# Kernel tuning notes

Hardware: AMD Instinct MI355X
Metric: run time of the kernel (lower is better)

The kernel has to match this reference:

```python
import jax, jax.numpy as jnp
import numpy as np

B = 128
J = 22
Q = J * 4          # 88
R = 3
C = 4
H = 512            # LSTM hidden
ENC = 256 * 3      # 768 concatenated encoder outputs
STATE_IN = Q + R + C   # 95
OFF_IN = Q + R         # 91
OUT = Q + R + C        # 95


def _linear_params(key, fan_in, fan_out):
    kw, kb = jax.random.split(key)
    s = 1.0 / np.sqrt(fan_in)
    w = jax.random.uniform(kw, (fan_in, fan_out), jnp.float32, -s, s)
    b = jax.random.uniform(kb, (fan_out,), jnp.float32, -s, s)
    return w, b


def setup_inputs() -> dict:
    key = jax.random.key(0)
    ks = jax.random.split(key, 24)
    inp = {
        "past_root_vel": jax.random.normal(ks[0], (B, 10, R)) * 0.1,
        "past_quats": jax.random.normal(ks[1], (B, 10, Q)),
        "past_root_offset": jax.random.normal(ks[2], (B, 10, R)),
        "past_quat_offset": jax.random.normal(ks[3], (B, 10, Q)),
        "past_contacts": jax.random.uniform(ks[4], (B, 10, C)),
        "target_root_pos": jax.random.normal(ks[5], (B, R)),
        "target_quats": jax.random.normal(ks[6], (B, Q)),
        "init_root_pos": jax.random.normal(ks[7], (B, R)),
        "pred_weights": jax.random.normal(ks[8], (B, 4 * H, ENC + H)) * 0.03,
        "pred_bias": jax.random.normal(ks[9], (B, 4 * H)) * 0.01,
    }
    inp["se_w1"], inp["se_b1"] = _linear_params(ks[10], STATE_IN, 512)
    inp["se_w2"], inp["se_b2"] = _linear_params(ks[11], 512, 256)
    inp["oe_w1"], inp["oe_b1"] = _linear_params(ks[12], OFF_IN, 512)
    inp["oe_w2"], inp["oe_b2"] = _linear_params(ks[13], 512, 256)
    inp["te_w1"], inp["te_b1"] = _linear_params(ks[14], Q, 512)
    inp["te_w2"], inp["te_b2"] = _linear_params(ks[15], 512, 256)
    inp["de_w1"], inp["de_b1"] = _linear_params(ks[16], H, 512)
    inp["de_w2"], inp["de_b2"] = _linear_params(ks[17], 512, 256)
    inp["de_w3"], inp["de_b3"] = _linear_params(ks[18], 256, OUT)
    return inp


def reference(past_root_vel, past_quats, past_root_offset, past_quat_offset,
              past_contacts, target_root_pos, target_quats, init_root_pos,
              pred_weights, pred_bias,
              se_w1, se_b1, se_w2, se_b2,
              oe_w1, oe_b1, oe_w2, oe_b2,
              te_w1, te_b1, te_w2, te_b2,
              de_w1, de_b1, de_w2, de_b2, de_w3, de_b3):
    b = past_quats.shape[0]

    def enc(x, w1, b1, w2, b2):
        return jax.nn.relu(jax.nn.relu(x @ w1 + b1) @ w2 + b2)

    # target encoding is identical every step; hoist it
    h_target = enc(target_quats, te_w1, te_b1, te_w2, te_b2)

    def step(root_vel, quats, root_offset, quat_offset, contacts, h, c):
        state_vec = jnp.concatenate([contacts, quats, root_vel], axis=1)
        offset_vec = jnp.concatenate([root_offset, quat_offset], axis=1)
        h_state = enc(state_vec, se_w1, se_b1, se_w2, se_b2)
        h_offset = enc(offset_vec, oe_w1, oe_b1, oe_w2, oe_b2)
        pred_in = jnp.concatenate([h_state, h_offset, h_target], axis=1)  # [B,768]
        # per-sample hypernetwork LSTM cell (torch gate order i,f,g,o)
        z = jnp.concatenate([pred_in, h], axis=1)  # [B, 1280]
        gates = jnp.einsum('boi,bi->bo', pred_weights, z) + pred_bias
        i_g, f_g, g_g, o_g = jnp.split(gates, 4, axis=1)
        c2 = jax.nn.sigmoid(f_g) * c + jax.nn.sigmoid(i_g) * jnp.tanh(g_g)
        h2 = jax.nn.sigmoid(o_g) * jnp.tanh(c2)
        # decoder (512,512,256,out), no activation on last layer
        d = jax.nn.relu(h2 @ de_w1 + de_b1)
        d = jax.nn.relu(d @ de_w2 + de_b2)
        out = d @ de_w3 + de_b3
        next_quats = out[:, :Q] + quats
        next_rvel = out[:, Q:Q + R] + root_vel
        next_contacts = jax.nn.sigmoid(out[:, Q + R:])
        nq = next_quats.reshape(b, Q // 4, 4)
        nq = nq / jnp.maximum(jnp.linalg.norm(nq, axis=2, keepdims=True), 1e-12)
        return next_rvel, nq.reshape(b, Q), next_contacts, h2, c2

    h0 = jnp.zeros((b, H), past_quats.dtype)
    c0 = jnp.zeros((b, H), past_quats.dtype)

    def past_body(carry, x):
        glob, h, c, _, _, _, _, _ = carry
        rvel, quats, roff, qoff, cont = x
        nrv, nq, nc, h2, c2 = step(rvel, quats, roff, qoff, cont, h, c)
        glob2 = glob + rvel
        nroff = glob2 - target_root_pos
        nqoff = nq - target_quats
        return (glob2, h2, c2, nrv, nq, nc, nroff, nqoff), None

    z3 = jnp.zeros((b, R), past_quats.dtype)
    init = (init_root_pos, h0, c0, z3,
            jnp.zeros((b, Q), past_quats.dtype),
            jnp.zeros((b, C), past_quats.dtype),
            z3, jnp.zeros((b, Q), past_quats.dtype))
    xs = (jnp.swapaxes(past_root_vel, 0, 1), jnp.swapaxes(past_quats, 0, 1),
          jnp.swapaxes(past_root_offset, 0, 1), jnp.swapaxes(past_quat_offset, 0, 1),
          jnp.swapaxes(past_contacts, 0, 1))
    carry, _ = jax.lax.scan(past_body, init, xs)
    glob, h, c, nrv, nq, nc, roff, qoff = carry

    first_frame = jnp.concatenate([nrv, nq], axis=1)  # NOTE: rvel not glob, as in source

    def trans_body(carry, _):
        glob, h, c, rvel, quats, cont, roff, qoff = carry
        nrv, nq, nc, h2, c2 = step(rvel, quats, roff, qoff, cont, h, c)
        glob2 = glob + nrv
        nroff = glob2 - target_root_pos
        nqoff = nq - target_quats
        pose = jnp.concatenate([glob2, nq], axis=1)
        return (glob2, h2, c2, nrv, nq, nc, nroff, nqoff), (pose, nc)

    carry2 = (glob, h, c, nrv, nq, nc, roff, qoff)
    _, (poses, conts) = jax.lax.scan(trans_body, carry2, None, length=29)

    pred_poses = jnp.concatenate([first_frame[:, None], jnp.swapaxes(poses, 0, 1)], axis=1)
    pred_contacts = jnp.concatenate([nc[:, None], jnp.swapaxes(conts, 0, 1)], axis=1)
    return pred_poses, pred_contacts
```

## Files before the change

kernel.cpp:

```cpp
#include <hip/hip_runtime.h>
#include <hip/hip_bf16.h>
#include <math.h>

#define BATCH 128
#define QD 88
#define HDIM 512
#define ZDIM 1280
#define GDIM 2048
#define PROW 1024
#define QSTRIDE 4096
#define NPAST 10
#define NTRANS 29
#define NSTEPS (NPAST + NTRANS)
#define OUTD 95
#define POSE_ELEMS (BATCH * 30 * 91)

typedef float f32x4 __attribute__((ext_vector_type(4)));
typedef unsigned int u32x4 __attribute__((ext_vector_type(4)));

__device__ __forceinline__ float sig_(float x) { return 1.0f / (1.0f + expf(-x)); }
__device__ __forceinline__ void dot4_(const u32x4 wv, const float4 zv, float& d) {
    const float4 f = *(const float4*)&wv;
    d = fmaf(f.x, zv.x, d); d = fmaf(f.y, zv.y, d);
    d = fmaf(f.z, zv.z, d); d = fmaf(f.w, zv.w, d);
}
__device__ __forceinline__ void dot4u_(const uint4 wv, const float4 zv, float& d) {
    const float4 f = *(const float4*)&wv;
    d = fmaf(f.x, zv.x, d); d = fmaf(f.y, zv.y, d);
    d = fmaf(f.z, zv.z, d); d = fmaf(f.w, zv.w, d);
}
__device__ __forceinline__ void fma4_(float4& acc, float x, const float4 w) {
    acc.x = fmaf(x, w.x, acc.x); acc.y = fmaf(x, w.y, acc.y);
    acc.z = fmaf(x, w.z, acc.z); acc.w = fmaf(x, w.w, acc.w);
}
__device__ __forceinline__ unsigned q8_(float w, float inv) {
    const unsigned u = __float2uint_rn(fmaf(w, inv, 128.0f));
    return (u > 255u) ? 255u : u;
}
__device__ __forceinline__ unsigned pack8_(const u32x4 a, float inv) {
    return q8_(__uint_as_float(a.x), inv) | (q8_(__uint_as_float(a.y), inv) << 8)
         | (q8_(__uint_as_float(a.z), inv) << 16) | (q8_(__uint_as_float(a.w), inv) << 24);
}
__device__ __forceinline__ float d8_(unsigned d, const float4 z) {
    float acc = 0.f;
    acc = fmaf((float)((int)(d & 0xFFu) - 128), z.x, acc);
    acc = fmaf((float)((int)((d >> 8) & 0xFFu) - 128), z.y, acc);
    acc = fmaf((float)((int)((d >> 16) & 0xFFu) - 128), z.z, acc);
    acc = fmaf((float)((int)(d >> 24) - 128), z.w, acc);
    return acc;
}
__device__ __forceinline__ float wredmax_(float m) {
    #pragma unroll
    for (int s = 32; s >= 1; s >>= 1) m = fmaxf(m, __shfl_xor(m, s, 64));
    return m;
}
__device__ __forceinline__ float amax4_(const u32x4 a, float m) {
    m = fmaxf(m, fabsf(__uint_as_float(a.x))); m = fmaxf(m, fabsf(__uint_as_float(a.y)));
    m = fmaxf(m, fabsf(__uint_as_float(a.z))); m = fmaxf(m, fabsf(__uint_as_float(a.w)));
    return m;
}

__global__ void __launch_bounds__(256)
matvec0_conv(const float* __restrict__ W, const float* __restrict__ z_ws,
             const float* __restrict__ pred_bias, unsigned char* __restrict__ Wp,
             float* __restrict__ scale_ws, float* __restrict__ g_ws, float* __restrict__ g0_ws)
{
    const int b = blockIdx.x >> 5, chunk = blockIdx.x & 31;
    const int wave = threadIdx.x >> 6, lane = threadIdx.x & 63;
    const int row0 = chunk * 64 + wave * 16;
    const float* zb = z_ws + b * ZDIM;
    const float biasv = (lane < 16) ? pred_bias[b * GDIM + row0 + lane] : 0.f;
    const int l4 = lane * 4;
    const float4 z0 = *(const float4*)(zb + l4);
    const float4 z1 = *(const float4*)(zb + 256 + l4);
    const float4 zh = *(const float4*)(zb + 512 + l4);
    const float4 z3 = *(const float4*)(zb + 768 + l4);
    const float4 z4 = *(const float4*)(zb + 1024 + l4);
    const char* wb = (const char*)W + (size_t)b * GDIM * ZDIM * 4;
    char* dstB = (char*)Wp + (size_t)b * GDIM * PROW;

    #define ISSUE(p, B) { const char* a_ = wb + (size_t)(row0 + 2 * (p)) * (ZDIM * 4) + lane * 16; \
        _Pragma("unroll") for (int i = 0; i < 10; ++i) \
            B[i] = __builtin_nontemporal_load((const u32x4*)(a_ + i * 1024)); }

    u32x4 bufa[10], bufb[10];
    ISSUE(0, bufa);
    #pragma unroll
    for (int p = 0; p < 8; ++p) {
        u32x4* cur = (p & 1) ? bufb : bufa;
        u32x4* nxt = (p & 1) ? bufa : bufb;
        if (p < 7) ISSUE(p + 1, nxt);
        float dynA = 0.f, dynB = 0.f, statA = 0.f, statB = 0.f;
        dot4_(cur[0], z0, dynA); dot4_(cur[1], z1, dynA);
        dot4_(cur[2], zh, statA);
        dot4_(cur[3], z3, dynA); dot4_(cur[4], z4, dynA);
        dot4_(cur[5], z0, dynB); dot4_(cur[6], z1, dynB);
        dot4_(cur[7], zh, statB);
        dot4_(cur[8], z3, dynB); dot4_(cur[9], z4, dynB);
        float m0 = 0.f, m1 = 0.f;
        m0 = amax4_(cur[0], m0); m0 = amax4_(cur[1], m0);
        m0 = amax4_(cur[3], m0); m0 = amax4_(cur[4], m0);
        m1 = amax4_(cur[5], m1); m1 = amax4_(cur[6], m1);
        m1 = amax4_(cur[8], m1); m1 = amax4_(cur[9], m1);
        m0 = wredmax_(m0); m1 = wredmax_(m1);
        const float s0 = m0 * (1.f / 127.f), s1 = m1 * (1.f / 127.f);
        const float inv0 = (m0 > 0.f) ? 127.f / m0 : 0.f;
        const float inv1 = (m1 > 0.f) ? 127.f / m1 : 0.f;
        {
            const int rp = row0 + 2 * p;
            char* base = dstB + (size_t)(rp >> 2) * QSTRIDE + (size_t)((rp >> 1) & 1) * 1024
                       + lane * 16;
            u32x4 v;
            v.x = pack8_(cur[0], inv0); v.y = pack8_(cur[1], inv0);
            v.z = pack8_(cur[5], inv1); v.w = pack8_(cur[6], inv1);
            __builtin_nontemporal_store(v, (u32x4*)(base));
            v.x = pack8_(cur[3], inv0); v.y = pack8_(cur[4], inv0);
            v.z = pack8_(cur[8], inv1); v.w = pack8_(cur[9], inv1);
            __builtin_nontemporal_store(v, (u32x4*)(base + 2048));
        }
        if (lane == 0) { scale_ws[b * GDIM + row0 + 2 * p] = s0;
                         scale_ws[b * GDIM + row0 + 2 * p + 1] = s1; }
        float sd0 = dynA + __shfl_xor(dynA, 32);
        float sd1 = dynB + __shfl_xor(dynB, 32);
        float ud = (lane < 32) ? sd0 : sd1;
        float ss0 = statA + __shfl_xor(statA, 32);
        float ss1 = statB + __shfl_xor(statB, 32);
        float us = (lane < 32) ? ss0 : ss1;
        #pragma unroll
        for (int m = 16; m >= 1; m >>= 1) { ud += __shfl_xor(ud, m); us += __shfl_xor(us, m); }
        const float badd = __shfl(biasv, 2 * p + ((lane >= 32) ? 1 : 0), 64);
        if (lane == 0 || lane == 32) {
            const int r = row0 + 2 * p + ((lane >= 32) ? 1 : 0);
            g0_ws[b * GDIM + r] = us + badd;
            g_ws[b * GDIM + r]  = ud + us + badd;
        }
    }
    #undef ISSUE
}

__device__ __forceinline__ void redwrite_(float rA, float rB, int lane,
                                          float g0v, float scv, int idx0,
                                          float* __restrict__ dst, int drow0) {
    const float sA = rA + __shfl_xor(rA, 32);
    const float sB = rB + __shfl_xor(rB, 32);
    float u = (lane < 32) ? sA : sB;
    #pragma unroll
    for (int m = 16; m >= 1; m >>= 1) u += __shfl_xor(u, m);
    const int hilo = (lane >= 32) ? 1 : 0;
    const float badd = __shfl(g0v, idx0 + hilo, 64);
    const float srow = __shfl(scv, idx0 + hilo, 64);
    const float val = badd + srow * u;
    if (lane == 0)       dst[drow0] = val;
    else if (lane == 32) dst[drow0 + 1] = val;
}

__global__ void __launch_bounds__(256)
epass(const unsigned char* __restrict__ Wp, const float* __restrict__ enc9,
      const float* __restrict__ scale_ws, const float* __restrict__ g0_ws,
      float* __restrict__ E_ws)
{
    const int b = blockIdx.x >> 5, chunk = blockIdx.x & 31;
    const int wave = threadIdx.x >> 6, lane = threadIdx.x & 63;
    const int row0 = chunk * 64 + wave * 16;
    const int q0 = row0 >> 2;
    const int l4 = lane * 4;
    float4 eA[9], eB[9];
    #pragma unroll
    for (int s = 0; s < 9; ++s) {
        const float* eb = enc9 + ((size_t)s * BATCH + b) * 512;
        eA[s] = *(const float4*)(eb + l4);
        eB[s] = *(const float4*)(eb + 256 + l4);
    }
    const float g0v = (lane < 16) ? g0_ws[b * GDIM + row0 + lane] : 0.f;
    const float scv = (lane < 16) ? scale_ws[b * GDIM + row0 + lane] : 0.f;
    const char* wb = (const char*)Wp + (size_t)b * GDIM * PROW;

    #define ISSUE(qq, B) { const char* a_ = wb + (size_t)(q0 + (qq)) * QSTRIDE + lane * 16; \
        B[0] = __builtin_nontemporal_load((const u32x4*)(a_)); \
        B[1] = __builtin_nontemporal_load((const u32x4*)(a_ + 1024)); }

    u32x4 bufa[2], bufb[2];
    ISSUE(0, bufa);
    #pragma unroll
    for (int qq = 0; qq < 4; ++qq) {
        u32x4* cur = (qq & 1) ? bufb : bufa;
        u32x4* nxt = (qq & 1) ? bufa : bufb;
        if (qq < 3) ISSUE(qq + 1, nxt);
        #pragma unroll
        for (int s = 0; s < 9; ++s) {
            const float r0 = d8_(cur[0].x, eA[s]) + d8_(cur[0].y, eB[s]);
            const float r1 = d8_(cur[0].z, eA[s]) + d8_(cur[0].w, eB[s]);
            const float r2 = d8_(cur[1].x, eA[s]) + d8_(cur[1].y, eB[s]);
            const float r3 = d8_(cur[1].z, eA[s]) + d8_(cur[1].w, eB[s]);
            float* dst = E_ws + ((size_t)s * BATCH + b) * GDIM;
            redwrite_(r0, r1, lane, g0v, scv, 4 * qq,     dst, row0 + 4 * qq);
            redwrite_(r2, r3, lane, g0v, scv, 4 * qq + 2, dst, row0 + 4 * qq + 2);
        }
    }
    #undef ISSUE
}

__global__ void __launch_bounds__(256)
matvecH(const unsigned char* __restrict__ Wp, const float* __restrict__ z_ws,
        const float* __restrict__ scale_ws, const float* __restrict__ Es,
        float* __restrict__ g_ws)
{
    const int b = blockIdx.x >> 5, chunk = blockIdx.x & 31;
    const int wave = threadIdx.x >> 6, lane = threadIdx.x & 63;
    const int row0 = chunk * 64 + wave * 16;
    const int q0 = row0 >> 2;
    const float* zb = z_ws + b * ZDIM;
    const int l4 = lane * 4;
    const float4 z3 = *(const float4*)(zb + 768 + l4);
    const float4 z4 = *(const float4*)(zb + 1024 + l4);
    const float Ev  = (lane < 16) ? Es[b * GDIM + row0 + lane] : 0.f;
    const float scv = (lane < 16) ? scale_ws[b * GDIM + row0 + lane] : 0.f;
    const char* wb = (const char*)Wp + (size_t)b * GDIM * PROW;

    #define ISSUE(qq, B) { const char* a_ = wb + (size_t)(q0 + (qq)) * QSTRIDE + 2048 + lane * 16; \
        B[0] = *(const u32x4*)(a_); \
        B[1] = *(const u32x4*)(a_ + 1024); }

    u32x4 buf0[2], buf1[2], buf2[2];
    ISSUE(0, buf0);
    ISSUE(1, buf1);
    #pragma unroll
    for (int qq = 0; qq < 4; ++qq) {
        u32x4* cur = (qq % 3 == 0) ? buf0 : (qq % 3 == 1) ? buf1 : buf2;
        u32x4* nxt = ((qq + 2) % 3 == 0) ? buf0 : ((qq + 2) % 3 == 1) ? buf1 : buf2;
        if (qq < 2) ISSUE(qq + 2, nxt);
        const float r0 = d8_(cur[0].x, z3) + d8_(cur[0].y, z4);
        const float r1 = d8_(cur[0].z, z3) + d8_(cur[0].w, z4);
        const float r2 = d8_(cur[1].x, z3) + d8_(cur[1].y, z4);
        const float r3 = d8_(cur[1].z, z3) + d8_(cur[1].w, z4);
        float* dst = g_ws + b * GDIM;
        redwrite_(r0, r1, lane, Ev, scv, 4 * qq,     dst, row0 + 4 * qq);
        redwrite_(r2, r3, lane, Ev, scv, 4 * qq + 2, dst, row0 + 4 * qq + 2);
    }
    #undef ISSUE
}

__global__ void __launch_bounds__(256)
matvec8(const unsigned char* __restrict__ Wp, const float* __restrict__ z_ws,
        const float* __restrict__ scale_ws, const float* __restrict__ g0_ws,
        float* __restrict__ g_ws)
{
    const int b = blockIdx.x >> 5, chunk = blockIdx.x & 31;
    const int wave = threadIdx.x >> 6, lane = threadIdx.x & 63;
    const int row0 = chunk * 64 + wave * 16;
    const int q0 = row0 >> 2;
    const float* zb = z_ws + b * ZDIM;
    const int l4 = lane * 4;
    const float4 z0 = *(const float4*)(zb + l4);
    const float4 z1 = *(const float4*)(zb + 256 + l4);
    const float4 z3 = *(const float4*)(zb + 768 + l4);
    const float4 z4 = *(const float4*)(zb + 1024 + l4);
    const float g0v = (lane < 16) ? g0_ws[b * GDIM + row0 + lane] : 0.f;
    const float scv = (lane < 16) ? scale_ws[b * GDIM + row0 + lane] : 0.f;
    const char* wb = (const char*)Wp + (size_t)b * GDIM * PROW;

    #define ISSUE(qq, B) { const char* a_ = wb + (size_t)(q0 + (qq)) * QSTRIDE + lane * 16; \
        B[0] = __builtin_nontemporal_load((const u32x4*)(a_)); \
        B[1] = __builtin_nontemporal_load((const u32x4*)(a_ + 1024)); \
        B[2] = __builtin_nontemporal_load((const u32x4*)(a_ + 2048)); \
        B[3] = __builtin_nontemporal_load((const u32x4*)(a_ + 3072)); }

    u32x4 buf0[4], buf1[4], buf2[4];
    ISSUE(0, buf0);
    ISSUE(1, buf1);
    #pragma unroll
    for (int qq = 0; qq < 4; ++qq) {
        u32x4* cur = (qq % 3 == 0) ? buf0 : (qq % 3 == 1) ? buf1 : buf2;
        u32x4* nxt = ((qq + 2) % 3 == 0) ? buf0 : ((qq + 2) % 3 == 1) ? buf1 : buf2;
        if (qq < 2) ISSUE(qq + 2, nxt);
        const float r0 = d8_(cur[0].x, z0) + d8_(cur[0].y, z1)
                       + d8_(cur[2].x, z3) + d8_(cur[2].y, z4);
        const float r1 = d8_(cur[0].z, z0) + d8_(cur[0].w, z1)
                       + d8_(cur[2].z, z3) + d8_(cur[2].w, z4);
        const float r2 = d8_(cur[1].x, z0) + d8_(cur[1].y, z1)
                       + d8_(cur[3].x, z3) + d8_(cur[3].y, z4);
        const float r3 = d8_(cur[1].z, z0) + d8_(cur[1].w, z1)
                       + d8_(cur[3].z, z3) + d8_(cur[3].w, z4);
        float* dst = g_ws + b * GDIM;
        redwrite_(r0, r1, lane, g0v, scv, 4 * qq,     dst, row0 + 4 * qq);
        redwrite_(r2, r3, lane, g0v, scv, 4 * qq + 2, dst, row0 + 4 * qq + 2);
    }
    #undef ISSUE
}

__global__ void __launch_bounds__(512)
lstmk(const float* __restrict__ g_ws, float* __restrict__ z_ws, float* __restrict__ c_ws)
{
    const int b = blockIdx.x, t = threadIdx.x;
    const float* g = g_ws + b * GDIM;
    const float ig = g[t], fg = g[512 + t], gg = g[1024 + t], og = g[1536 + t];
    const float c2 = sig_(fg) * c_ws[b * HDIM + t] + sig_(ig) * tanhf(gg);
    c_ws[b * HDIM + t] = c2;
    z_ws[b * ZDIM + 768 + t] = sig_(og) * tanhf(c2);
}

__global__ void __launch_bounds__(512)
initk(const float* __restrict__ past_root_vel, const float* __restrict__ past_quats,
      const float* __restrict__ past_root_offset, const float* __restrict__ past_quat_offset,
      const float* __restrict__ past_contacts, const float* __restrict__ target_quats,
      const float* __restrict__ init_root_pos,
      const float* __restrict__ se_w1, const float* __restrict__ se_b1,
      const float* __restrict__ se_w2, const float* __restrict__ se_b2,
      const float* __restrict__ oe_w1, const float* __restrict__ oe_b1,
      const float* __restrict__ oe_w2, const float* __restrict__ oe_b2,
      const float* __restrict__ te_w1, const float* __restrict__ te_b1,
      const float* __restrict__ te_w2, const float* __restrict__ te_b2,
      float* __restrict__ z_ws, float* __restrict__ c_ws, float* __restrict__ car_ws)
{
    const int b = blockIdx.x, t = threadIdx.x;
    __shared__ float tq[QD], bufA[512], bufB[512], sv[95], ov[91];

    if (t < 192) {
        float v = 0.f;
        if (t < 3) {
            v = init_root_pos[b * 3 + t];
            for (int s = 0; s < NPAST - 1; ++s) v += past_root_vel[(b * NPAST + s) * 3 + t];
        }
        car_ws[b * 192 + t] = v;
    }
    c_ws[b * HDIM + t] = 0.f;
    z_ws[b * ZDIM + 768 + t] = 0.f;
    if (t < QD) tq[t] = target_quats[b * QD + t];
    if (t < 4)  sv[t] = past_contacts[b * NPAST * 4 + t];
    if (t < QD) { sv[4 + t] = past_quats[b * NPAST * QD + t];
                  ov[3 + t] = past_quat_offset[b * NPAST * QD + t]; }
    if (t < 3)  { sv[92 + t] = past_root_vel[b * NPAST * 3 + t];
                  ov[t]      = past_root_offset[b * NPAST * 3 + t]; }
    __syncthreads();
    {
        float a = te_b1[t];
        #pragma unroll 8
        for (int i = 0; i < QD; ++i) a = fmaf(tq[i], te_w1[i * 512 + t], a);
        bufA[t] = fmaxf(a, 0.f);
    }
    __syncthreads();
    if (t < 256) {
        float a = te_b2[t];
        #pragma unroll 8
        for (int i = 0; i < 512; ++i) a = fmaf(bufA[i], te_w2[i * 256 + t], a);
        z_ws[b * ZDIM + 512 + t] = fmaxf(a, 0.f);
    }
    __syncthreads();
    {
        float aS = se_b1[t], aO = oe_b1[t];
        #pragma unroll 8
        for (int i = 0; i < 91; ++i) { aS = fmaf(sv[i], se_w1[i * 512 + t], aS);
                                       aO = fmaf(ov[i], oe_w1[i * 512 + t], aO); }
        #pragma unroll
        for (int i = 91; i < 95; ++i) aS = fmaf(sv[i], se_w1[i * 512 + t], aS);
        bufA[t] = fmaxf(aS, 0.f);
        bufB[t] = fmaxf(aO, 0.f);
    }
    __syncthreads();
    if (t < 256) {
        float a = se_b2[t];
        #pragma unroll 8
        for (int i = 0; i < 512; ++i) a = fmaf(bufA[i], se_w2[i * 256 + t], a);
        z_ws[b * ZDIM + t] = fmaxf(a, 0.f);
    } else {
        const int j = t - 256;
        float a = oe_b2[j];
        #pragma unroll 8
        for (int i = 0; i < 512; ++i) a = fmaf(bufB[i], oe_w2[i * 256 + j], a);
        z_ws[b * ZDIM + 256 + j] = fmaxf(a, 0.f);
    }
}

__global__ void __launch_bounds__(512)
enc_past(const float* __restrict__ past_root_vel, const float* __restrict__ past_quats,
         const float* __restrict__ past_root_offset, const float* __restrict__ past_quat_offset,
         const float* __restrict__ past_contacts,
         const float* __restrict__ se_w1, const float* __restrict__ se_b1,
         const float* __restrict__ se_w2, const float* __restrict__ se_b2,
         const float* __restrict__ oe_w1, const float* __restrict__ oe_b1,
         const float* __restrict__ oe_w2, const float* __restrict__ oe_b2,
         float* __restrict__ enc9)
{
    const int b = blockIdx.x, t = threadIdx.x;
    const int s = blockIdx.y + 1;
    __shared__ float bufA[512], bufB[512], sv[95], ov[91];

    if (t < 4)  sv[t] = past_contacts[(b * NPAST + s) * 4 + t];
    if (t < QD) { sv[4 + t] = past_quats[(b * NPAST + s) * QD + t];
                  ov[3 + t] = past_quat_offset[(b * NPAST + s) * QD + t]; }
    if (t < 3)  { sv[92 + t] = past_root_vel[(b * NPAST + s) * 3 + t];
                  ov[t]      = past_root_offset[(b * NPAST + s) * 3 + t]; }
    __syncthreads();
    {
        float aS = se_b1[t], aO = oe_b1[t];
        #pragma unroll 8
        for (int i = 0; i < 91; ++i) { aS = fmaf(sv[i], se_w1[i * 512 + t], aS);
                                       aO = fmaf(ov[i], oe_w1[i * 512 + t], aO); }
        #pragma unroll
        for (int i = 91; i < 95; ++i) aS = fmaf(sv[i], se_w1[i * 512 + t], aS);
        bufA[t] = fmaxf(aS, 0.f);
        bufB[t] = fmaxf(aO, 0.f);
    }
    __syncthreads();
    float* dst = enc9 + ((size_t)(s - 1) * BATCH + b) * 512;
    if (t < 256) {
        float a = se_b2[t];
        #pragma unroll 8
        for (int i = 0; i < 512; ++i) a = fmaf(bufA[i], se_w2[i * 256 + t], a);
        dst[t] = fmaxf(a, 0.f);
    } else {
        const int j = t - 256;
        float a = oe_b2[j];
        #pragma unroll 8
        for (int i = 0; i < 512; ++i) a = fmaf(bufB[i], oe_w2[i * 256 + j], a);
        dst[256 + j] = fmaxf(a, 0.f);
    }
}

__global__ void __launch_bounds__(512)
stepk(const float* __restrict__ past_root_vel, const float* __restrict__ past_quats,
      const float* __restrict__ past_root_offset, const float* __restrict__ past_quat_offset,
      const float* __restrict__ past_contacts, const float* __restrict__ target_root_pos,
      const float* __restrict__ target_quats,
      const float* __restrict__ se_w1, const float* __restrict__ se_b1,
      const float* __restrict__ se_w2, const float* __restrict__ se_b2,
      const float* __restrict__ oe_w1, const float* __restrict__ oe_b1,
      const float* __restrict__ oe_w2, const float* __restrict__ oe_b2,
      const float* __restrict__ de_w1, const float* __restrict__ de_b1,
      const float* __restrict__ de_w2, const float* __restrict__ de_b2,
      const float* __restrict__ de_w3, const float* __restrict__ de_b3,
      float* __restrict__ out, float* __restrict__ z_ws, const float* __restrict__ g_ws,
      float* __restrict__ c_ws, float* __restrict__ car_ws, int s, int skip_enc)
{
    const int b = blockIdx.x, t = threadIdx.x;
    __shared__ float4 part4[512];
    __shared__ __align__(16) float h2s[HDIM], bufA[512], bufB[512], d2[256];
    __shared__ float outv[OUTD], nq[QD], sv[95], ov[91], carryL[192], tq[QD], trp[3];
    __shared__ float rvn[3], globn[3], contn[4];

    if (t < 192) carryL[t] = car_ws[b * 192 + t];
    if (t < QD) tq[t] = target_quats[b * QD + t];
    if (t < 3)  trp[t] = target_root_pos[b * 3 + t];

    {
        const float* g = g_ws + b * GDIM;
        const float ig = g[t], fg = g[512 + t], gg = g[1024 + t], og = g[1536 + t];
        const float c2 = sig_(fg) * c_ws[b * HDIM + t] + sig_(ig) * tanhf(gg);
        c_ws[b * HDIM + t] = c2;
        const float h2 = sig_(og) * tanhf(c2);
        h2s[t] = h2;
        z_ws[b * ZDIM + 768 + t] = h2;
    }
    __syncthreads();
    {
        const int c = t & 127, s4 = t >> 7;
        float4 acc = {0.f, 0.f, 0.f, 0.f};
        const float* w = de_w1 + (size_t)(s4 * 128) * 512 + 4 * c;
        #pragma unroll 8
        for (int k = 0; k < 128; ++k)
            fma4_(acc, h2s[s4 * 128 + k], *(const float4*)(w + (size_t)k * 512));
        part4[t] = acc;
    }
    __syncthreads();
    if (t < 128) {
        float4 v = part4[t];
        #pragma unroll
        for (int s4 = 1; s4 < 4; ++s4) { const float4 p = part4[s4 * 128 + t];
            v.x += p.x; v.y += p.y; v.z += p.z; v.w += p.w; }
        const float4 bb = *(const float4*)(de_b1 + 4 * t);
        float4 r; r.x = fmaxf(v.x + bb.x, 0.f); r.y = fmaxf(v.y + bb.y, 0.f);
        r.z = fmaxf(v.z + bb.z, 0.f); r.w = fmaxf(v.w + bb.w, 0.f);
        *(float4*)&bufA[4 * t] = r;
    }
    __syncthreads();
    {
        const int c = t & 63, s8 = t >> 6;
        float4 acc = {0.f, 0.f, 0.f, 0.f};
        const float* w = de_w2 + (size_t)(s8 * 64) * 256 + 4 * c;
        #pragma unroll 8
        for (int k = 0; k < 64; ++k)
            fma4_(acc, bufA[s8 * 64 + k], *(const float4*)(w + (size_t)k * 256));
        part4[t] = acc;
    }
    __syncthreads();
    if (t < 64) {
        float4 v = part4[t];
        #pragma unroll
        for (int s8 = 1; s8 < 8; ++s8) { const float4 p = part4[s8 * 64 + t];
            v.x += p.x; v.y += p.y; v.z += p.z; v.w += p.w; }
        const float4 bb = *(const float4*)(de_b2 + 4 * t);
        float4 r; r.x = fmaxf(v.x + bb.x, 0.f); r.y = fmaxf(v.y + bb.y, 0.f);
        r.z = fmaxf(v.z + bb.z, 0.f); r.w = fmaxf(v.w + bb.w, 0.f);
        *(float4*)&d2[4 * t] = r;
    }
    __syncthreads();
    if (t < OUTD) {
        float acc = de_b3[t];
        #pragma unroll 16
        for (int i = 0; i < 256; ++i) acc = fmaf(d2[i], de_w3[i * OUTD + t], acc);
        outv[t] = acc;
    }
    __syncthreads();

    const bool pastS = (s < NPAST);
    if (t < QD) {
        const float qin = pastS ? past_quats[(b * NPAST + s) * QD + t] : carryL[10 + t];
        nq[t] = outv[t] + qin;
    }
    __syncthreads();
    if (t < 22) {
        const float a = nq[4 * t], b2 = nq[4 * t + 1], c3 = nq[4 * t + 2], d4 = nq[4 * t + 3];
        const float inv = 1.f / fmaxf(sqrtf(a * a + b2 * b2 + c3 * c3 + d4 * d4), 1e-12f);
        nq[4 * t] = a * inv; nq[4 * t + 1] = b2 * inv; nq[4 * t + 2] = c3 * inv; nq[4 * t + 3] = d4 * inv;
    }
    if (t < 3) {
        const float rin = pastS ? past_root_vel[(b * NPAST + s) * 3 + t] : carryL[3 + t];
        const float nrv = outv[88 + t] + rin;
        const float g = carryL[t] + (pastS ? rin : nrv);
        rvn[t] = nrv; globn[t] = g;
    }
    if (t < 4) contn[t] = sig_(outv[91 + t]);
    __syncthreads();

    if (t < 3) { car_ws[b * 192 + t] = globn[t]; car_ws[b * 192 + 3 + t] = rvn[t];
                 car_ws[b * 192 + 186 + t] = globn[t] - trp[t]; }
    if (t < 4) car_ws[b * 192 + 6 + t] = contn[t];
    if (t < QD) { car_ws[b * 192 + 10 + t] = nq[t]; car_ws[b * 192 + 98 + t] = nq[t] - tq[t]; }
    if (s == NPAST - 1) {
        const size_t pb = (size_t)b * 30 * 91;
        if (t < 3)  out[pb + t] = rvn[t];
        if (t < QD) out[pb + 3 + t] = nq[t];
        if (t < 4)  out[POSE_ELEMS + (size_t)b * 30 * 4 + t] = contn[t];
    } else if (!pastS) {
        const int k = s - NPAST + 1;
        const size_t pb = ((size_t)b * 30 + k) * 91;
        if (t < 3)  out[pb + t] = globn[t];
        if (t < QD) out[pb + 3 + t] = nq[t];
        if (t < 4)  out[POSE_ELEMS + ((size_t)b * 30 + k) * 4 + t] = contn[t];
    }
    if (s == NSTEPS - 1) return;
    if (skip_enc) return;

    const int nx = s + 1;
    if (nx < NPAST) {
        if (t < 4)  sv[t] = past_contacts[(b * NPAST + nx) * 4 + t];
        if (t < QD) { sv[4 + t] = past_quats[(b * NPAST + nx) * QD + t];
                      ov[3 + t] = past_quat_offset[(b * NPAST + nx) * QD + t]; }
        if (t < 3)  { sv[92 + t] = past_root_vel[(b * NPAST + nx) * 3 + t];
                      ov[t]      = past_root_offset[(b * NPAST + nx) * 3 + t]; }
    } else {
        if (t < 4)  sv[t] = contn[t];
        if (t < QD) { sv[4 + t] = nq[t]; ov[3 + t] = nq[t] - tq[t]; }
        if (t < 3)  { sv[92 + t] = rvn[t]; ov[t] = globn[t] - trp[t]; }
    }
    __syncthreads();
    {
        const int tt = t & 255, enc = t >> 8;
        const int c = tt & 127, sl = tt >> 7;
        const float* inp = enc ? ov : sv;
        const float* w1  = enc ? oe_w1 : se_w1;
        const int nin  = enc ? 91 : 95;
        const int half = enc ? 46 : 48;
        const int i0 = sl * half;
        const int iend = (i0 + half < nin) ? (i0 + half) : nin;
        float4 acc = {0.f, 0.f, 0.f, 0.f};
        #pragma unroll 8
        for (int k = 0; k < 48; ++k) {
            const int i = i0 + k;
            if (i < iend) fma4_(acc, inp[i], *(const float4*)(w1 + (size_t)i * 512 + 4 * c));
        }
        part4[enc * 256 + tt] = acc;
    }
    __syncthreads();
    if (t < 128) {
        const float4 a = part4[t], b2 = part4[128 + t];
        const float4 bb = *(const float4*)(se_b1 + 4 * t);
        float4 r; r.x = fmaxf(a.x + b2.x + bb.x, 0.f); r.y = fmaxf(a.y + b2.y + bb.y, 0.f);
        r.z = fmaxf(a.z + b2.z + bb.z, 0.f); r.w = fmaxf(a.w + b2.w + bb.w, 0.f);
        *(float4*)&bufA[4 * t] = r;
    } else if (t < 256) {
        const int c = t - 128;
        const float4 a = part4[256 + c], b2 = part4[384 + c];
        const float4 bb = *(const float4*)(oe_b1 + 4 * c);
        float4 r; r.x = fmaxf(a.x + b2.x + bb.x, 0.f); r.y = fmaxf(a.y + b2.y + bb.y, 0.f);
        r.z = fmaxf(a.z + b2.z + bb.z, 0.f); r.w = fmaxf(a.w + b2.w + bb.w, 0.f);
        *(float4*)&bufB[4 * c] = r;
    }
    __syncthreads();
    {
        const int tt = t & 255, enc = t >> 8;
        const int c = tt & 63, sl = tt >> 6;
        const float* inp = enc ? bufB : bufA;
        const float* w2  = enc ? oe_w2 : se_w2;
        float4 acc = {0.f, 0.f, 0.f, 0.f};
        const float* w = w2 + (size_t)(sl * 128) * 256 + 4 * c;
        #pragma unroll 8
        for (int k = 0; k < 128; ++k)
            fma4_(acc, inp[sl * 128 + k], *(const float4*)(w + (size_t)k * 256));
        part4[enc * 256 + tt] = acc;
    }
    __syncthreads();
    if (t < 64) {
        float4 v = part4[t];
        #pragma unroll
        for (int sl = 1; sl < 4; ++sl) { const float4 p = part4[sl * 64 + t];
            v.x += p.x; v.y += p.y; v.z += p.z; v.w += p.w; }
        const float4 bb = *(const float4*)(se_b2 + 4 * t);
        float4 r; r.x = fmaxf(v.x + bb.x, 0.f); r.y = fmaxf(v.y + bb.y, 0.f);
        r.z = fmaxf(v.z + bb.z, 0.f); r.w = fmaxf(v.w + bb.w, 0.f);
        *(float4*)(z_ws + b * ZDIM + 4 * t) = r;
    } else if (t < 128) {
        const int c = t - 64;
        float4 v = part4[256 + c];
        #pragma unroll
        for (int sl = 1; sl < 4; ++sl) { const float4 p = part4[256 + sl * 64 + c];
            v.x += p.x; v.y += p.y; v.z += p.z; v.w += p.w; }
        const float4 bb = *(const float4*)(oe_b2 + 4 * c);
        float4 r; r.x = fmaxf(v.x + bb.x, 0.f); r.y = fmaxf(v.y + bb.y, 0.f);
        r.z = fmaxf(v.z + bb.z, 0.f); r.w = fmaxf(v.w + bb.w, 0.f);
        *(float4*)(z_ws + b * ZDIM + 256 + 4 * c) = r;
    }
}

__global__ void __launch_bounds__(256)
matvec_f32(const float* __restrict__ W, const float* __restrict__ z_ws,
           const float* __restrict__ pred_bias, float* __restrict__ g_ws)
{
    const int b = blockIdx.x >> 5, chunk = blockIdx.x & 31;
    const int wave = threadIdx.x >> 6, lane = threadIdx.x & 63;
    const int row0 = chunk * 64 + wave * 16;
    const float* zb = z_ws + b * ZDIM;
    const float biasv = (lane < 16) ? pred_bias[b * GDIM + row0 + lane] : 0.f;
    const int l4 = lane * 4;
    const float4 z0 = *(const float4*)(zb + l4);
    const float4 z1 = *(const float4*)(zb + 256 + l4);
    const float4 z2 = *(const float4*)(zb + 512 + l4);
    const float4 z3 = *(const float4*)(zb + 768 + l4);
    const float4 z4 = *(const float4*)(zb + 1024 + l4);
    const char* wb = (const char*)W + (size_t)b * GDIM * ZDIM * 4;

    #define ISSUE(p, B) { const char* a_ = wb + (size_t)(row0 + 2 * (p)) * (ZDIM * 4) + lane * 16; \
        _Pragma("unroll") for (int i = 0; i < 10; ++i) B[i] = *(const uint4*)(a_ + i * 1024); }

    uint4 bufa[10], bufb[10];
    ISSUE(0, bufa);
    #pragma unroll
    for (int p = 0; p < 8; ++p) {
        uint4* cur = (p & 1) ? bufb : bufa;
        uint4* nxt = (p & 1) ? bufa : bufb;
        if (p < 7) ISSUE(p + 1, nxt);
        float accA = 0.f, accB = 0.f;
        dot4u_(cur[0], z0, accA); dot4u_(cur[1], z1, accA); dot4u_(cur[2], z2, accA);
        dot4u_(cur[3], z3, accA); dot4u_(cur[4], z4, accA);
        dot4u_(cur[5], z0, accB); dot4u_(cur[6], z1, accB); dot4u_(cur[7], z2, accB);
        dot4u_(cur[8], z3, accB); dot4u_(cur[9], z4, accB);
        float s0 = accA + __shfl_xor(accA, 32);
        float s1 = accB + __shfl_xor(accB, 32);
        float u = (lane < 32) ? s0 : s1;
        #pragma unroll
        for (int m = 16; m >= 1; m >>= 1) u += __shfl_xor(u, m);
        const float badd = __shfl(biasv, 2 * p + ((lane >= 32) ? 1 : 0), 64);
        if (lane == 0)       g_ws[b * GDIM + row0 + 2 * p]     = u + badd;
        else if (lane == 32) g_ws[b * GDIM + row0 + 2 * p + 1] = u + badd;
    }
    #undef ISSUE
}

extern "C" void kernel_launch(void* const* d_in, const int* in_sizes, int n_in,
                              void* d_out, int out_size, void* d_ws, size_t ws_size,
                              hipStream_t stream) {
    const float* prv = (const float*)d_in[0];
    const float* pq  = (const float*)d_in[1];
    const float* pro = (const float*)d_in[2];
    const float* pqo = (const float*)d_in[3];
    const float* pc  = (const float*)d_in[4];
    const float* trp = (const float*)d_in[5];
    const float* tq  = (const float*)d_in[6];
    const float* irp = (const float*)d_in[7];
    const float* pw  = (const float*)d_in[8];
    const float* pb  = (const float*)d_in[9];
    const float* se_w1 = (const float*)d_in[10]; const float* se_b1 = (const float*)d_in[11];
    const float* se_w2 = (const float*)d_in[12]; const float* se_b2 = (const float*)d_in[13];
    const float* oe_w1 = (const float*)d_in[14]; const float* oe_b1 = (const float*)d_in[15];
    const float* oe_w2 = (const float*)d_in[16]; const float* oe_b2 = (const float*)d_in[17];
    const float* te_w1 = (const float*)d_in[18]; const float* te_b1 = (const float*)d_in[19];
    const float* te_w2 = (const float*)d_in[20]; const float* te_b2 = (const float*)d_in[21];
    const float* de_w1 = (const float*)d_in[22]; const float* de_b1 = (const float*)d_in[23];
    const float* de_w2 = (const float*)d_in[24]; const float* de_b2 = (const float*)d_in[25];
    const float* de_w3 = (const float*)d_in[26]; const float* de_b3 = (const float*)d_in[27];
    float* outp = (float*)d_out;

    const size_t WPACKB = (size_t)BATCH * GDIM * PROW;
    const size_t AUXB = (size_t)BATCH * (GDIM * 3 + ZDIM + HDIM + 192) * 4
                      + (size_t)9 * BATCH * 512 * 4
                      + (size_t)9 * BATCH * GDIM * 4;
    const bool bf = ws_size >= WPACKB + AUXB;

    char* base = (char*)d_ws;
    float* scale_ws; float* g0_ws; float* z_ws;
    if (bf) {
        scale_ws = (float*)(base + WPACKB);
        g0_ws    = scale_ws + (size_t)BATCH * GDIM;
        z_ws     = g0_ws + (size_t)BATCH * GDIM;
    } else {
        scale_ws = nullptr;
        g0_ws    = nullptr;
        z_ws     = (float*)base;
    }
    float* g_ws    = z_ws + (size_t)BATCH * ZDIM;
    float* c_ws    = g_ws + (size_t)BATCH * GDIM;
    float* car_ws  = c_ws + (size_t)BATCH * HDIM;
    float* enc9_ws = car_ws + (size_t)BATCH * 192;
    float* E_ws    = enc9_ws + (size_t)9 * BATCH * 512;

    initk<<<dim3(BATCH), dim3(512), 0, stream>>>(prv, pq, pro, pqo, pc, tq, irp,
        se_w1, se_b1, se_w2, se_b2, oe_w1, oe_b1, oe_w2, oe_b2,
        te_w1, te_b1, te_w2, te_b2, z_ws, c_ws, car_ws);

    if (bf) {
        enc_past<<<dim3(BATCH, 9), dim3(512), 0, stream>>>(prv, pq, pro, pqo, pc,
            se_w1, se_b1, se_w2, se_b2, oe_w1, oe_b1, oe_w2, oe_b2, enc9_ws);
        matvec0_conv<<<dim3(BATCH * 32), dim3(256), 0, stream>>>(
            pw, z_ws, pb, (unsigned char*)d_ws, scale_ws, g_ws, g0_ws);
        epass<<<dim3(BATCH * 32), dim3(256), 0, stream>>>(
            (const unsigned char*)d_ws, enc9_ws, scale_ws, g0_ws, E_ws);
        for (int s = 0; s < NSTEPS; ++s) {
            if (s >= 1 && s < NPAST) {
                matvecH<<<dim3(BATCH * 32), dim3(256), 0, stream>>>(
                    (const unsigned char*)d_ws, z_ws, scale_ws,
                    E_ws + (size_t)(s - 1) * BATCH * GDIM, g_ws);
            } else if (s >= NPAST) {
                matvec8<<<dim3(BATCH * 32), dim3(256), 0, stream>>>(
                    (const unsigned char*)d_ws, z_ws, scale_ws, g0_ws, g_ws);
            }
            if (s < NPAST - 1) {
                lstmk<<<dim3(BATCH), dim3(512), 0, stream>>>(g_ws, z_ws, c_ws);
            } else {
                stepk<<<dim3(BATCH), dim3(512), 0, stream>>>(prv, pq, pro, pqo, pc, trp, tq,
                    se_w1, se_b1, se_w2, se_b2, oe_w1, oe_b1, oe_w2, oe_b2,
                    de_w1, de_b1, de_w2, de_b2, de_w3, de_b3,
                    outp, z_ws, g_ws, c_ws, car_ws, s, 0);
            }
        }
    } else {
        for (int s = 0; s < NSTEPS; ++s) {
            matvec_f32<<<dim3(BATCH * 32), dim3(256), 0, stream>>>(pw, z_ws, pb, g_ws);
            stepk<<<dim3(BATCH), dim3(512), 0, stream>>>(prv, pq, pro, pqo, pc, trp, tq,
                se_w1, se_b1, se_w2, se_b2, oe_w1, oe_b1, oe_w2, oe_b2,
                de_w1, de_b1, de_w2, de_b2, de_w3, de_b3,
                outp, z_ws, g_ws, c_ws, car_ws, s, 0);
        }
    }
}
```

Before: 3.418 ms.

## Split transition matvec into hidden and state parts, overlap decoder tail with hidden matvec

In the transition phase, the single fused matvec over the state, offset and hidden parts is split in two. The hidden-state part (matvecH, writing partial gates to a scratch buffer) runs in the same launch as the per-batch decoder/encoder tail (bck). A smaller matvecS then adds the state-encoder contribution once the tail has produced the new encodings. The intent is to take the decoder MLP and state-encoder work off the serial critical path by running it concurrently with the large weight stream, at the cost of an extra launch per step and a read/write of the partial gate buffer. matvecH loads also switch to nontemporal.

```diff
diff --git a/kernel.cpp b/kernel.cpp
--- a/kernel.cpp
+++ b/kernel.cpp
@@ -200,13 +200,14 @@
     #undef ISSUE
 }
 
-__global__ void __launch_bounds__(256)
-matvecH(const unsigned char* __restrict__ Wp, const float* __restrict__ z_ws,
-        const float* __restrict__ scale_ws, const float* __restrict__ Es,
-        float* __restrict__ g_ws)
-{
-    const int b = blockIdx.x >> 5, chunk = blockIdx.x & 31;
-    const int wave = threadIdx.x >> 6, lane = threadIdx.x & 63;
+__device__ __forceinline__ void mvH_body_(int blk, const unsigned char* __restrict__ Wp,
+                                          const float* __restrict__ z_ws,
+                                          const float* __restrict__ scale_ws,
+                                          const float* __restrict__ Es,
+                                          float* __restrict__ dstg, int tid)
+{
+    const int b = blk >> 5, chunk = blk & 31;
+    const int wave = tid >> 6, lane = tid & 63;
     const int row0 = chunk * 64 + wave * 16;
     const int q0 = row0 >> 2;
     const float* zb = z_ws + b * ZDIM;
@@ -218,8 +219,8 @@
     const char* wb = (const char*)Wp + (size_t)b * GDIM * PROW;
 
     #define ISSUE(qq, B) { const char* a_ = wb + (size_t)(q0 + (qq)) * QSTRIDE + 2048 + lane * 16; \
-        B[0] = *(const u32x4*)(a_); \
-        B[1] = *(const u32x4*)(a_ + 1024); }
+        B[0] = __builtin_nontemporal_load((const u32x4*)(a_)); \
+        B[1] = __builtin_nontemporal_load((const u32x4*)(a_ + 1024)); }
 
     u32x4 buf0[2], buf1[2], buf2[2];
     ISSUE(0, buf0);
@@ -233,7 +234,7 @@
         const float r1 = d8_(cur[0].z, z3) + d8_(cur[0].w, z4);
         const float r2 = d8_(cur[1].x, z3) + d8_(cur[1].y, z4);
         const float r3 = d8_(cur[1].z, z3) + d8_(cur[1].w, z4);
-        float* dst = g_ws + b * GDIM;
+        float* dst = dstg + b * GDIM;
         redwrite_(r0, r1, lane, Ev, scv, 4 * qq,     dst, row0 + 4 * qq);
         redwrite_(r2, r3, lane, Ev, scv, 4 * qq + 2, dst, row0 + 4 * qq + 2);
     }
@@ -241,8 +242,16 @@
 }
 
 __global__ void __launch_bounds__(256)
-matvec8(const unsigned char* __restrict__ Wp, const float* __restrict__ z_ws,
-        const float* __restrict__ scale_ws, const float* __restrict__ g0_ws,
+matvecH(const unsigned char* __restrict__ Wp, const float* __restrict__ z_ws,
+        const float* __restrict__ scale_ws, const float* __restrict__ Es,
+        float* __restrict__ g_ws)
+{
+    mvH_body_(blockIdx.x, Wp, z_ws, scale_ws, Es, g_ws, threadIdx.x);
+}
+
+__global__ void __launch_bounds__(256)
+matvecS(const unsigned char* __restrict__ Wp, const float* __restrict__ z_ws,
+        const float* __restrict__ scale_ws, const float* __restrict__ Es,
         float* __restrict__ g_ws)
 {
     const int b = blockIdx.x >> 5, chunk = blockIdx.x & 31;
@@ -253,19 +262,15 @@
     const int l4 = lane * 4;
     const float4 z0 = *(const float4*)(zb + l4);
     const float4 z1 = *(const float4*)(zb + 256 + l4);
-    const float4 z3 = *(const float4*)(zb + 768 + l4);
-    const float4 z4 = *(const float4*)(zb + 1024 + l4);
-    const float g0v = (lane < 16) ? g0_ws[b * GDIM + row0 + lane] : 0.f;
+    const float Ev  = (lane < 16) ? Es[b * GDIM + row0 + lane] : 0.f;
     const float scv = (lane < 16) ? scale_ws[b * GDIM + row0 + lane] : 0.f;
     const char* wb = (const char*)Wp + (size_t)b * GDIM * PROW;
 
     #define ISSUE(qq, B) { const char* a_ = wb + (size_t)(q0 + (qq)) * QSTRIDE + lane * 16; \
         B[0] = __builtin_nontemporal_load((const u32x4*)(a_)); \
-        B[1] = __builtin_nontemporal_load((const u32x4*)(a_ + 1024)); \
-        B[2] = __builtin_nontemporal_load((const u32x4*)(a_ + 2048)); \
-        B[3] = __builtin_nontemporal_load((const u32x4*)(a_ + 3072)); }
-
-    u32x4 buf0[4], buf1[4], buf2[4];
+        B[1] = __builtin_nontemporal_load((const u32x4*)(a_ + 1024)); }
+
+    u32x4 buf0[2], buf1[2], buf2[2];
     ISSUE(0, buf0);
     ISSUE(1, buf1);
     #pragma unroll
@@ -273,17 +278,13 @@
         u32x4* cur = (qq % 3 == 0) ? buf0 : (qq % 3 == 1) ? buf1 : buf2;
         u32x4* nxt = ((qq + 2) % 3 == 0) ? buf0 : ((qq + 2) % 3 == 1) ? buf1 : buf2;
         if (qq < 2) ISSUE(qq + 2, nxt);
-        const float r0 = d8_(cur[0].x, z0) + d8_(cur[0].y, z1)
-                       + d8_(cur[2].x, z3) + d8_(cur[2].y, z4);
-        const float r1 = d8_(cur[0].z, z0) + d8_(cur[0].w, z1)
-                       + d8_(cur[2].z, z3) + d8_(cur[2].w, z4);
-        const float r2 = d8_(cur[1].x, z0) + d8_(cur[1].y, z1)
-                       + d8_(cur[3].x, z3) + d8_(cur[3].y, z4);
-        const float r3 = d8_(cur[1].z, z0) + d8_(cur[1].w, z1)
-                       + d8_(cur[3].z, z3) + d8_(cur[3].w, z4);
+        const float r0 = d8_(cur[0].x, z0) + d8_(cur[0].y, z1);
+        const float r1 = d8_(cur[0].z, z0) + d8_(cur[0].w, z1);
+        const float r2 = d8_(cur[1].x, z0) + d8_(cur[1].y, z1);
+        const float r3 = d8_(cur[1].z, z0) + d8_(cur[1].w, z1);
         float* dst = g_ws + b * GDIM;
-        redwrite_(r0, r1, lane, g0v, scv, 4 * qq,     dst, row0 + 4 * qq);
-        redwrite_(r2, r3, lane, g0v, scv, 4 * qq + 2, dst, row0 + 4 * qq + 2);
+        redwrite_(r0, r1, lane, Ev, scv, 4 * qq,     dst, row0 + 4 * qq);
+        redwrite_(r2, r3, lane, Ev, scv, 4 * qq + 2, dst, row0 + 4 * qq + 2);
     }
     #undef ISSUE
 }
@@ -297,6 +298,193 @@
     const float c2 = sig_(fg) * c_ws[b * HDIM + t] + sig_(ig) * tanhf(gg);
     c_ws[b * HDIM + t] = c2;
     z_ws[b * ZDIM + 768 + t] = sig_(og) * tanhf(c2);
+}
+
+__device__ void btail_(int b, int t, int s, int do_enc,
+                       const float* __restrict__ target_root_pos,
+                       const float* __restrict__ target_quats,
+                       const float* __restrict__ se_w1, const float* __restrict__ se_b1,
+                       const float* __restrict__ se_w2, const float* __restrict__ se_b2,
+                       const float* __restrict__ oe_w1, const float* __restrict__ oe_b1,
+                       const float* __restrict__ oe_w2, const float* __restrict__ oe_b2,
+                       const float* __restrict__ de_w1, const float* __restrict__ de_b1,
+                       const float* __restrict__ de_w2, const float* __restrict__ de_b2,
+                       const float* __restrict__ de_w3, const float* __restrict__ de_b3,
+                       float* __restrict__ out, float* __restrict__ z_ws,
+                       float* __restrict__ car_ws)
+{
+    __shared__ float4 part4[256];
+    __shared__ __align__(16) float h2s[HDIM], bufA[512], bufB[512], d2[256];
+    __shared__ float outv[OUTD], nq[QD], sv[95], ov[91], carryL[192], tq[QD], trp[3];
+    __shared__ float rvn[3], globn[3], contn[4];
+
+    if (t < 192) carryL[t] = car_ws[b * 192 + t];
+    if (t < QD) tq[t] = target_quats[b * QD + t];
+    if (t < 3)  trp[t] = target_root_pos[b * 3 + t];
+    h2s[t] = z_ws[b * ZDIM + 768 + t];
+    h2s[256 + t] = z_ws[b * ZDIM + 768 + 256 + t];
+    __syncthreads();
+
+    {
+        const int c = t & 127, sl = t >> 7;
+        float4 acc = {0.f, 0.f, 0.f, 0.f};
+        const float* w = de_w1 + (size_t)(sl * 256) * 512 + 4 * c;
+        #pragma unroll 8
+        for (int k = 0; k < 256; ++k)
+            fma4_(acc, h2s[sl * 256 + k], *(const float4*)(w + (size_t)k * 512));
+        part4[t] = acc;
+    }
+    __syncthreads();
+    if (t < 128) {
+        const float4 a = part4[t], b2 = part4[128 + t];
+        const float4 bb = *(const float4*)(de_b1 + 4 * t);
+        float4 r; r.x = fmaxf(a.x + b2.x + bb.x, 0.f); r.y = fmaxf(a.y + b2.y + bb.y, 0.f);
+        r.z = fmaxf(a.z + b2.z + bb.z, 0.f); r.w = fmaxf(a.w + b2.w + bb.w, 0.f);
+        *(float4*)&bufA[4 * t] = r;
+    }
+    __syncthreads();
+    {
+        const int c = t & 63, sl = t >> 6;
+        float4 acc = {0.f, 0.f, 0.f, 0.f};
+        const float* w = de_w2 + (size_t)(sl * 128) * 256 + 4 * c;
+        #pragma unroll 8
+        for (int k = 0; k < 128; ++k)
+            fma4_(acc, bufA[sl * 128 + k], *(const float4*)(w + (size_t)k * 256));
+        part4[t] = acc;
+    }
+    __syncthreads();
+    if (t < 64) {
+        float4 v = part4[t];
+        #pragma unroll
+        for (int sl = 1; sl < 4; ++sl) { const float4 p = part4[sl * 64 + t];
+            v.x += p.x; v.y += p.y; v.z += p.z; v.w += p.w; }
+        const float4 bb = *(const float4*)(de_b2 + 4 * t);
+        float4 r; r.x = fmaxf(v.x + bb.x, 0.f); r.y = fmaxf(v.y + bb.y, 0.f);
+        r.z = fmaxf(v.z + bb.z, 0.f); r.w = fmaxf(v.w + bb.w, 0.f);
+        *(float4*)&d2[4 * t] = r;
+    }
+    __syncthreads();
+    if (t < OUTD) {
+        float acc = de_b3[t];
+        #pragma unroll 16
+        for (int i = 0; i < 256; ++i) acc = fmaf(d2[i], de_w3[i * OUTD + t], acc);
+        outv[t] = acc;
+    }
+    __syncthreads();
+
+    if (t < QD) nq[t] = outv[t] + carryL[10 + t];
+    __syncthreads();
+    if (t < 22) {
+        const float a = nq[4 * t], b2 = nq[4 * t + 1], c3 = nq[4 * t + 2], d4 = nq[4 * t + 3];
+        const float inv = 1.f / fmaxf(sqrtf(a * a + b2 * b2 + c3 * c3 + d4 * d4), 1e-12f);
+        nq[4 * t] = a * inv; nq[4 * t + 1] = b2 * inv; nq[4 * t + 2] = c3 * inv; nq[4 * t + 3] = d4 * inv;
+    }
+    if (t < 3) {
+        const float nrv = outv[88 + t] + carryL[3 + t];
+        const float g = carryL[t] + nrv;
+        rvn[t] = nrv; globn[t] = g;
+    }
+    if (t < 4) contn[t] = sig_(outv[91 + t]);
+    __syncthreads();
+
+    if (t < 3) { car_ws[b * 192 + t] = globn[t]; car_ws[b * 192 + 3 + t] = rvn[t];
+                 car_ws[b * 192 + 186 + t] = globn[t] - trp[t]; }
+    if (t < 4) car_ws[b * 192 + 6 + t] = contn[t];
+    if (t < QD) { car_ws[b * 192 + 10 + t] = nq[t]; car_ws[b * 192 + 98 + t] = nq[t] - tq[t]; }
+    {
+        const int k = s - NPAST + 1;
+        const size_t pb = ((size_t)b * 30 + k) * 91;
+        if (t < 3)  out[pb + t] = globn[t];
+        if (t < QD) out[pb + 3 + t] = nq[t];
+        if (t < 4)  out[POSE_ELEMS + ((size_t)b * 30 + k) * 4 + t] = contn[t];
+    }
+    if (!do_enc) return;
+
+    if (t < 4)  sv[t] = contn[t];
+    if (t < QD) { sv[4 + t] = nq[t]; ov[3 + t] = nq[t] - tq[t]; }
+    if (t < 3)  { sv[92 + t] = rvn[t]; ov[t] = globn[t] - trp[t]; }
+    __syncthreads();
+    {
+        const int enc = t >> 7, c = t & 127;
+        const float* inp = enc ? ov : sv;
+        const float* w1  = enc ? oe_w1 : se_w1;
+        const float* b1  = enc ? oe_b1 : se_b1;
+        const int nin = enc ? 91 : 95;
+        float4 acc = {0.f, 0.f, 0.f, 0.f};
+        for (int i = 0; i < nin; ++i)
+            fma4_(acc, inp[i], *(const float4*)(w1 + (size_t)i * 512 + 4 * c));
+        const float4 bb = *(const float4*)(b1 + 4 * c);
+        float4 r; r.x = fmaxf(acc.x + bb.x, 0.f); r.y = fmaxf(acc.y + bb.y, 0.f);
+        r.z = fmaxf(acc.z + bb.z, 0.f); r.w = fmaxf(acc.w + bb.w, 0.f);
+        if (enc) *(float4*)&bufB[4 * c] = r; else *(float4*)&bufA[4 * c] = r;
+    }
+    __syncthreads();
+    {
+        const int enc = t >> 7, tt = t & 127;
+        const int c = tt & 63, sl = tt >> 6;
+        const float* inp = enc ? bufB : bufA;
+        const float* w2  = enc ? oe_w2 : se_w2;
+        float4 acc = {0.f, 0.f, 0.f, 0.f};
+        const float* w = w2 + (size_t)(sl * 256) * 256 + 4 * c;
+        #pragma unroll 8
+        for (int k = 0; k < 256; ++k)
+            fma4_(acc, inp[sl * 256 + k], *(const float4*)(w + (size_t)k * 256));
+        part4[t] = acc;
+    }
+    __syncthreads();
+    if (t < 64) {
+        const float4 a = part4[t], b2 = part4[64 + t];
+        const float4 bb = *(const float4*)(se_b2 + 4 * t);
+        float4 r; r.x = fmaxf(a.x + b2.x + bb.x, 0.f); r.y = fmaxf(a.y + b2.y + bb.y, 0.f);
+        r.z = fmaxf(a.z + b2.z + bb.z, 0.f); r.w = fmaxf(a.w + b2.w + bb.w, 0.f);
+        *(float4*)(z_ws + b * ZDIM + 4 * t) = r;
+    } else if (t < 128) {
+        const int c = t - 64;
+        const float4 a = part4[128 + c], b2 = part4[192 + c];
+        const float4 bb = *(const float4*)(oe_b2 + 4 * c);
+        float4 r; r.x = fmaxf(a.x + b2.x + bb.x, 0.f); r.y = fmaxf(a.y + b2.y + bb.y, 0.f);
+        r.z = fmaxf(a.z + b2.z + bb.z, 0.f); r.w = fmaxf(a.w + b2.w + bb.w, 0.f);
+        *(float4*)(z_ws + b * ZDIM + 256 + 4 * c) = r;
+    }
+}
+
+__global__ void __launch_bounds__(256)
+bck(const unsigned char* __restrict__ Wp, float* __restrict__ z_ws,
+    const float* __restrict__ scale_ws, const float* __restrict__ g0_ws,
+    float* __restrict__ gpart,
+    const float* __restrict__ target_root_pos, const float* __restrict__ target_quats,
+    const float* __restrict__ se_w1, const float* __restrict__ se_b1,
+    const float* __restrict__ se_w2, const float* __restrict__ se_b2,
+    const float* __restrict__ oe_w1, const float* __restrict__ oe_b1,
+    const float* __restrict__ oe_w2, const float* __restrict__ oe_b2,
+    const float* __restrict__ de_w1, const float* __restrict__ de_b1,
+    const float* __restrict__ de_w2, const float* __restrict__ de_b2,
+    const float* __restrict__ de_w3, const float* __restrict__ de_b3,
+    float* __restrict__ out, float* __restrict__ car_ws, int s)
+{
+    if (blockIdx.x < BATCH) {
+        btail_(blockIdx.x, threadIdx.x, s, 1, target_root_pos, target_quats,
+               se_w1, se_b1, se_w2, se_b2, oe_w1, oe_b1, oe_w2, oe_b2,
+               de_w1, de_b1, de_w2, de_b2, de_w3, de_b3, out, z_ws, car_ws);
+    } else {
+        mvH_body_(blockIdx.x - BATCH, Wp, z_ws, scale_ws, g0_ws, gpart, threadIdx.x);
+    }
+}
+
+__global__ void __launch_bounds__(256)
+tailk(const float* __restrict__ target_root_pos, const float* __restrict__ target_quats,
+      const float* __restrict__ se_w1, const float* __restrict__ se_b1,
+      const float* __restrict__ se_w2, const float* __restrict__ se_b2,
+      const float* __restrict__ oe_w1, const float* __restrict__ oe_b1,
+      const float* __restrict__ oe_w2, const float* __restrict__ oe_b2,
+      const float* __restrict__ de_w1, const float* __restrict__ de_b1,
+      const float* __restrict__ de_w2, const float* __restrict__ de_b2,
+      const float* __restrict__ de_w3, const float* __restrict__ de_b3,
+      float* __restrict__ out, float* __restrict__ z_ws, float* __restrict__ car_ws, int s)
+{
+    btail_(blockIdx.x, threadIdx.x, s, 0, target_root_pos, target_quats,
+           se_w1, se_b1, se_w2, se_b2, oe_w1, oe_b1, oe_w2, oe_b2,
+           de_w1, de_b1, de_w2, de_b2, de_w3, de_b3, out, z_ws, car_ws);
 }
 
 __global__ void __launch_bounds__(512)
@@ -724,22 +912,36 @@
             pw, z_ws, pb, (unsigned char*)d_ws, scale_ws, g_ws, g0_ws);
         epass<<<dim3(BATCH * 32), dim3(256), 0, stream>>>(
             (const unsigned char*)d_ws, enc9_ws, scale_ws, g0_ws, E_ws);
-        for (int s = 0; s < NSTEPS; ++s) {
-            if (s >= 1 && s < NPAST) {
+        for (int s = 0; s < NPAST; ++s) {
+            if (s >= 1)
                 matvecH<<<dim3(BATCH * 32), dim3(256), 0, stream>>>(
                     (const unsigned char*)d_ws, z_ws, scale_ws,
                     E_ws + (size_t)(s - 1) * BATCH * GDIM, g_ws);
-            } else if (s >= NPAST) {
-                matvec8<<<dim3(BATCH * 32), dim3(256), 0, stream>>>(
-                    (const unsigned char*)d_ws, z_ws, scale_ws, g0_ws, g_ws);
-            }
-            if (s < NPAST - 1) {
+            if (s < NPAST - 1)
                 lstmk<<<dim3(BATCH), dim3(512), 0, stream>>>(g_ws, z_ws, c_ws);
-            } else {
+            else
                 stepk<<<dim3(BATCH), dim3(512), 0, stream>>>(prv, pq, pro, pqo, pc, trp, tq,
                     se_w1, se_b1, se_w2, se_b2, oe_w1, oe_b1, oe_w2, oe_b2,
                     de_w1, de_b1, de_w2, de_b2, de_w3, de_b3,
                     outp, z_ws, g_ws, c_ws, car_ws, s, 0);
+        }
+        matvecH<<<dim3(BATCH * 32), dim3(256), 0, stream>>>(
+            (const unsigned char*)d_ws, z_ws, scale_ws, g0_ws, E_ws);
+        matvecS<<<dim3(BATCH * 32), dim3(256), 0, stream>>>(
+            (const unsigned char*)d_ws, z_ws, scale_ws, E_ws, g_ws);
+        for (int s = NPAST; s < NSTEPS; ++s) {
+            lstmk<<<dim3(BATCH), dim3(512), 0, stream>>>(g_ws, z_ws, c_ws);
+            if (s < NSTEPS - 1) {
+                bck<<<dim3(BATCH * 32 + BATCH), dim3(256), 0, stream>>>(
+                    (const unsigned char*)d_ws, z_ws, scale_ws, g0_ws, E_ws,
+                    trp, tq, se_w1, se_b1, se_w2, se_b2, oe_w1, oe_b1, oe_w2, oe_b2,
+                    de_w1, de_b1, de_w2, de_b2, de_w3, de_b3, outp, car_ws, s);
+                matvecS<<<dim3(BATCH * 32), dim3(256), 0, stream>>>(
+                    (const unsigned char*)d_ws, z_ws, scale_ws, E_ws, g_ws);
+            } else {
+                tailk<<<dim3(BATCH), dim3(256), 0, stream>>>(
+                    trp, tq, se_w1, se_b1, se_w2, se_b2, oe_w1, oe_b1, oe_w2, oe_b2,
+                    de_w1, de_b1, de_w2, de_b2, de_w3, de_b3, outp, z_ws, car_ws, s);
             }
         }
     } else {
```

After: 4.120 ms. +20.5%, slower.
